# Kernel tuning notes

Hardware: AMD Instinct MI355X
Metric: run time of the kernel (lower is better)

## Reference

```python
import jax, jax.numpy as jnp
import numpy as np

B, C, H, W = 8, 256, 128, 128

def setup_inputs() -> dict:
    key = jax.random.key(0)
    k1, k2 = jax.random.split(key)
    x = jax.random.normal(k1, (B, C, H, W), dtype=jnp.float32)
    # guide is a per-pixel gate map (broadcast over channels), values in [0, 1)
    guide = jax.random.uniform(k2, (B, 1, H, W), dtype=jnp.float32)
    return {"x": x, "guide": guide}

def reference(x, guide):
    # guide.expand_as(x): broadcast the [B,1,H,W] gate over channels
    g = jnp.broadcast_to(guide, x.shape)
    gated = x * g  # guide-modulated features
    # Guided directional max pool: running max along W (left -> right),
    # i.e. out[..., t] = max_{j <= t} (x * guide)[..., j].
    # associative_scan with jnp.maximum is the exact, differentiable cummax;
    # the argmax index ('maxout' in the CUDA op) is implicit in autodiff.
    out = jax.lax.associative_scan(jnp.maximum, gated, axis=-1)
    return out
```

## Files before the change

kernel.cpp:

```cpp
#include <hip/hip_runtime.h>

#define PB 8
#define PC 256
#define PH 128
#define PW 128

__global__ __launch_bounds__(256) void i5pool_cummax_kernel(
    const float* __restrict__ x,
    const float* __restrict__ guide,
    float* __restrict__ out)
{
    const int tid = blockIdx.x * blockDim.x + threadIdx.x;
    const int sub = tid & 31;
    const int row = tid >> 5;

    const int h  = row & (PH - 1);
    const int bc = row >> 7;
    const int b  = bc >> 8;

    const float4* xr = (const float4*)(x + (size_t)row * PW) + sub;
    const float4* gr = (const float4*)(guide + ((size_t)b * PH + h) * PW) + sub;

    float4 xv = *xr;
    float4 gv = *gr;

    float s0 = xv.x * gv.x;
    float s1 = fmaxf(s0, xv.y * gv.y);
    float s2 = fmaxf(s1, xv.z * gv.z);
    float s3 = fmaxf(s2, xv.w * gv.w);

    float inc = s3;
    #pragma unroll
    for (int d = 1; d < 32; d <<= 1) {
        float t = __shfl_up(inc, d, 32);
        if (sub >= d) inc = fmaxf(inc, t);
    }
    float pre = __shfl_up(inc, 1, 32);
    if (sub > 0) {
        s0 = fmaxf(s0, pre);
        s1 = fmaxf(s1, pre);
        s2 = fmaxf(s2, pre);
        s3 = fmaxf(s3, pre);
    }

    float4 ov = make_float4(s0, s1, s2, s3);
    *((float4*)(out + (size_t)row * PW) + sub) = ov;
}

extern "C" void kernel_launch(void* const* d_in, const int* in_sizes, int n_in,
                              void* d_out, int out_size, void* d_ws, size_t ws_size,
                              hipStream_t stream) {
    const float* x     = (const float*)d_in[0];
    const float* guide = (const float*)d_in[1];
    float* out = (float*)d_out;

    const int total_threads = PB * PC * PH * (PW / 4);
    const int block = 256;
    const int grid = total_threads / block;

    i5pool_cummax_kernel<<<grid, block, 0, stream>>>(x, guide, out);
}
```

Before: 222.6 us.

## Process four rows per thread with nontemporal loads and stores

Each thread now handles four rows spaced a quarter of the tensor apart, which gives it four independent loads in flight and lets the four shuffle scans interleave. The x loads and output stores use nontemporal builtins to avoid polluting the cache with streaming data. The grid shrinks by four, which trades fewer waves and less latency hiding from occupancy for more per-thread memory-level parallelism. Guide reads remain cached, and the four rows per thread likely fall in different batches, so guide reuse across threads is unchanged.

```diff
diff --git a/kernel.cpp b/kernel.cpp
--- a/kernel.cpp
+++ b/kernel.cpp
@@ -4,47 +4,67 @@
 #define PC 256
 #define PH 128
 #define PW 128
+#define TOTAL_ROWS (PB * PC * PH)
+#define QROWS (TOTAL_ROWS / 4)
+
+typedef float vfloat4 __attribute__((ext_vector_type(4)));
 
 __global__ __launch_bounds__(256) void i5pool_cummax_kernel(
     const float* __restrict__ x,
     const float* __restrict__ guide,
     float* __restrict__ out)
 {
-    const int tid = blockIdx.x * blockDim.x + threadIdx.x;
-    const int sub = tid & 31;
-    const int row = tid >> 5;
+    const int tid   = blockIdx.x * blockDim.x + threadIdx.x;
+    const int sub   = tid & 31;
+    const int rbase = tid >> 5;
 
-    const int h  = row & (PH - 1);
-    const int bc = row >> 7;
-    const int b  = bc >> 8;
+    int rows[4];
+    #pragma unroll
+    for (int i = 0; i < 4; ++i) rows[i] = rbase + i * QROWS;
 
-    const float4* xr = (const float4*)(x + (size_t)row * PW) + sub;
-    const float4* gr = (const float4*)(guide + ((size_t)b * PH + h) * PW) + sub;
+    vfloat4 xv[4], gv[4];
+    #pragma unroll
+    for (int i = 0; i < 4; ++i) {
+        const int r = rows[i];
+        const int h = r & (PH - 1);
+        const int b = r >> 15;
+        xv[i] = __builtin_nontemporal_load((const vfloat4*)(x + (size_t)r * PW) + sub);
+        gv[i] = *((const vfloat4*)(guide + ((size_t)b * PH + h) * PW) + sub);
+    }
 
-    float4 xv = *xr;
-    float4 gv = *gr;
+    float s[4][4];
+    #pragma unroll
+    for (int i = 0; i < 4; ++i) {
+        s[i][0] = xv[i].x * gv[i].x;
+        s[i][1] = fmaxf(s[i][0], xv[i].y * gv[i].y);
+        s[i][2] = fmaxf(s[i][1], xv[i].z * gv[i].z);
+        s[i][3] = fmaxf(s[i][2], xv[i].w * gv[i].w);
+    }
 
-    float s0 = xv.x * gv.x;
-    float s1 = fmaxf(s0, xv.y * gv.y);
-    float s2 = fmaxf(s1, xv.z * gv.z);
-    float s3 = fmaxf(s2, xv.w * gv.w);
-
-    float inc = s3;
+    float inc[4];
+    #pragma unroll
+    for (int i = 0; i < 4; ++i) inc[i] = s[i][3];
     #pragma unroll
     for (int d = 1; d < 32; d <<= 1) {
-        float t = __shfl_up(inc, d, 32);
-        if (sub >= d) inc = fmaxf(inc, t);
-    }
-    float pre = __shfl_up(inc, 1, 32);
-    if (sub > 0) {
-        s0 = fmaxf(s0, pre);
-        s1 = fmaxf(s1, pre);
-        s2 = fmaxf(s2, pre);
-        s3 = fmaxf(s3, pre);
+        float t[4];
+        #pragma unroll
+        for (int i = 0; i < 4; ++i) t[i] = __shfl_up(inc[i], d, 32);
+        if (sub >= d) {
+            #pragma unroll
+            for (int i = 0; i < 4; ++i) inc[i] = fmaxf(inc[i], t[i]);
+        }
     }
 
-    float4 ov = make_float4(s0, s1, s2, s3);
-    *((float4*)(out + (size_t)row * PW) + sub) = ov;
+    #pragma unroll
+    for (int i = 0; i < 4; ++i) {
+        float pre = __shfl_up(inc[i], 1, 32);
+        if (sub > 0) {
+            #pragma unroll
+            for (int j = 0; j < 4; ++j) s[i][j] = fmaxf(s[i][j], pre);
+        }
+        vfloat4 ov = {s[i][0], s[i][1], s[i][2], s[i][3]};
+        __builtin_nontemporal_store(ov, (vfloat4*)(out + (size_t)rows[i] * PW) + sub);
+    }
 }
 
 extern "C" void kernel_launch(void* const* d_in, const int* in_sizes, int n_in,
@@ -54,7 +74,7 @@
     const float* guide = (const float*)d_in[1];
     float* out = (float*)d_out;
 
-    const int total_threads = PB * PC * PH * (PW / 4);
+    const int total_threads = QROWS * (PW / 4);
     const int block = 256;
     const int grid = total_threads / block;
 
```

After: 226.0 us. Within noise of the previous version (+1.5%).
